# Kernel optimization log

Hardware: AMD Instinct MI355X
Metric: run time of the kernel (lower is better)

Reference implementation:

```python
import jax, jax.numpy as jnp
import numpy as np

K = 9          # neighbors kept after dilation
DILATION = 2   # top-k runs with K*DILATION then strided slice
EPS = 1e-12    # F.normalize eps


def setup_inputs() -> dict:
    key = jax.random.key(0)
    # x: [B, C, N, 1] feature map over N points with C channels
    x = jax.random.normal(key, (2, 64, 8192, 1), dtype=jnp.float32)
    return {"x": x}


def reference(x):
    k_total = K * DILATION
    # L2-normalize along channel dim (F.normalize(x, p=2, dim=1))
    norm = jnp.sqrt(jnp.sum(x * x, axis=1, keepdims=True))
    xn = x / jnp.maximum(norm, EPS)
    # [B, C, N, 1] -> [B, N, C]
    pts = jnp.transpose(jnp.squeeze(xn, -1), (0, 2, 1))
    B, N, _ = pts.shape
    # pairwise squared distances: ||xi||^2 - 2 xi.xj + ||xj||^2  -> [B, N, N]
    sq = jnp.sum(pts * pts, axis=-1, keepdims=True)            # [B, N, 1]
    dist = sq - 2.0 * jnp.einsum('bnc,bmc->bnm', pts, pts) + jnp.swapaxes(sq, 1, 2)
    # k nearest = top-k of negated distance (matches torch.topk(-dist, k))
    _, nn_idx = jax.lax.top_k(-dist, k_total)                  # [B, N, k_total] int32
    center_idx = jnp.broadcast_to(jnp.arange(N, dtype=nn_idx.dtype)[None, :, None],
                                  (B, N, k_total))
    edge_index = jnp.stack([nn_idx, center_idx], axis=0)       # [2, B, N, k_total]
    # dilation (non-stochastic path): strided slice over neighbor dim
    return edge_index[:, :, :, ::DILATION]                     # [2, B, N, K]
```

## Files before the change

kernel.cpp:

```cpp
#include <hip/hip_runtime.h>


#define NPTS  8192
#define CHN   64
#define NB    2
#define KF    18
#define KC    8
#define KM    16
#define KOUT  9
#define NPART 4
#define TPB   32

typedef unsigned u32;
typedef unsigned short u16;
typedef unsigned long long u64;
typedef __attribute__((ext_vector_type(4))) unsigned u32x4;
typedef __attribute__((ext_vector_type(8))) short bf16x8;
typedef __attribute__((ext_vector_type(4))) float f32x4;

__device__ __forceinline__ u32 umin32(u32 a, u32 b) { return a < b ? a : b; }

__device__ __forceinline__ u32 mono32(float f) {
  const u32 u = __float_as_uint(f);
  const u32 s = (u32)((int)u >> 31);
  return u ^ (s | 0x80000000u);
}

__device__ __forceinline__ u32 med3u(u32 a, u32 b, u32 c) {
  u32 r;
  asm("v_med3_u32 %0, %1, %2, %3" : "=v"(r) : "v"(a), "v"(b), "v"(c));
  return r;
}

template <int KK>
__device__ __forceinline__ void insmm(u32 key, u32 (&d)[KK]) {
#pragma unroll
  for (int k = KK - 1; k >= 1; --k) d[k] = med3u(d[k - 1], d[k], key);
  d[0] = umin32(d[0], key);
}

template <int KK>
__device__ __forceinline__ void ins64(u64 key, u64 (&d)[KK]) {
  if (key < d[KK - 1]) {
#pragma unroll
    for (int k = KK - 1; k >= 1; --k) {
      const bool up = d[k - 1] > key;
      const bool here = (!up) && (d[k] > key);
      d[k] = up ? d[k - 1] : (here ? key : d[k]);
    }
    if (d[0] > key) d[0] = key;
  }
}

__device__ __forceinline__ void gload_lds16(const u32* g, u32* l) {
  __builtin_amdgcn_global_load_lds(
      (const __attribute__((address_space(1))) u32*)g,
      (__attribute__((address_space(3))) u32*)l, 16, 0, 0);
}

__device__ __forceinline__ void np_normalize(const float* __restrict__ xb,
                                             float (&v)[CHN]) {
  float ss = 0.f;
#pragma unroll
  for (int c = 0; c < CHN; ++c) {
    v[c] = xb[(size_t)c * NPTS];
    ss = __fadd_rn(ss, __fmul_rn(v[c], v[c]));
  }
  const float den = fmaxf(__fsqrt_rn(ss), 1e-12f);
#pragma unroll
  for (int c = 0; c < CHN; ++c) v[c] = __fdiv_rn(v[c], den);
}

__global__ __launch_bounds__(128) void prep_kernel(
    const float* __restrict__ x, u32* __restrict__ hib, u32* __restrict__ lob,
    u32* __restrict__ w16b, float* __restrict__ sq) {
  const int b = blockIdx.x >> 6;
  const int n = ((blockIdx.x & 63) << 7) + threadIdx.x;
  const int g = (b << 13) + n;
  float v[CHN];
  np_normalize(x + (size_t)b * CHN * NPTS + n, v);
  float r[8];
#pragma unroll
  for (int j = 0; j < 8; ++j) r[j] = __fmul_rn(v[j], v[j]);
#pragma unroll
  for (int blk = 1; blk < 8; ++blk)
#pragma unroll
    for (int j = 0; j < 8; ++j)
      r[j] = __fadd_rn(r[j], __fmul_rn(v[8 * blk + j], v[8 * blk + j]));
  const float t0 = __fadd_rn(r[0], r[1]);
  const float t1 = __fadd_rn(r[2], r[3]);
  const float t2 = __fadd_rn(r[4], r[5]);
  const float t3 = __fadd_rn(r[6], r[7]);
  sq[g] = __fadd_rn(__fadd_rn(t0, t1), __fadd_rn(t2, t3));
  u32* hd = hib + (size_t)g * 32;
  u32* ld = lob + (size_t)g * 32;
  u32* wd = w16b + (size_t)g * 32;
  const int key = n & 7;
#pragma unroll
  for (int q = 0; q < 8; ++q) {
    u32 h[4], l[4], w[4];
#pragma unroll
    for (int p2 = 0; p2 < 4; ++p2) {
      const float a = v[8 * q + 2 * p2];
      const float c = v[8 * q + 2 * p2 + 1];
      const u32 ba = __float_as_uint(a), bc = __float_as_uint(c);
      const float la = a - __uint_as_float(ba & 0xffff0000u);
      const float lc = c - __uint_as_float(bc & 0xffff0000u);
      h[p2] = __builtin_amdgcn_perm(bc, ba, 0x07060302u);
      l[p2] = __builtin_amdgcn_perm(__float_as_uint(lc), __float_as_uint(la),
                                    0x07060302u);
      w[p2] = __builtin_amdgcn_perm(bc, ba, 0x05040100u);
    }
    const int pq = (q ^ key) << 2;
    *(u32x4*)(hd + pq) = (u32x4){h[0], h[1], h[2], h[3]};
    *(u32x4*)(ld + pq) = (u32x4){l[0], l[1], l[2], l[3]};
    *(u32x4*)(wd + pq) = (u32x4){w[0], w[1], w[2], w[3]};
  }
}

__global__ __launch_bounds__(256, 2) void knn_part_kernel(
    const u32* __restrict__ hib, const u32* __restrict__ lob,
    const float* __restrict__ sq, u16* __restrict__ cand) {
  __shared__ __align__(16) u32 pw[4][2][2048];

  const int tid = threadIdx.x;
  const int vb = ((blockIdx.x & 7) << 7) + (blockIdx.x >> 3);
  const int part = vb >> 8;
  const int w = vb & 255;
  const int b = w >> 7;
  const int qbase = (w & 127) << 6;
  const int t_lo = part << 5;
  const u32* __restrict__ hb_ = hib + ((size_t)b << 18);
  const u32* __restrict__ lb_ = lob + ((size_t)b << 18);
  const float* __restrict__ sqb = sq + (b << 13);

  const int lane = tid & 63, wid = tid >> 6;
  const int qoff = (wid & 1) << 5;
  const int moff = (wid >> 1) << 5;
  const int l15 = lane & 15;
  const int h4 = lane >> 4;
  const int sw = l15 & 7;
  const int lofs = lane << 2;

#define STAGE(BUF, TILE)                                                     \
  {                                                                          \
    const u32* sH_ = hb_ + ((size_t)(TILE) << 11) + (moff << 5);             \
    const u32* sL_ = lb_ + ((size_t)(TILE) << 11) + (moff << 5);             \
    u32* bp_ = &pw[wid][(BUF)][0];                                           \
    gload_lds16(sH_ + lofs, bp_ + lofs);                                     \
    gload_lds16(sH_ + 256 + lofs, bp_ + 256 + lofs);                         \
    gload_lds16(sH_ + 512 + lofs, bp_ + 512 + lofs);                         \
    gload_lds16(sH_ + 768 + lofs, bp_ + 768 + lofs);                         \
    gload_lds16(sL_ + lofs, bp_ + 1024 + lofs);                              \
    gload_lds16(sL_ + 256 + lofs, bp_ + 1280 + lofs);                        \
    gload_lds16(sL_ + 512 + lofs, bp_ + 1536 + lofs);                        \
    gload_lds16(sL_ + 768 + lofs, bp_ + 1792 + lofs);                        \
  }

  STAGE(0, t_lo)
  float sqn0 = sqb[(t_lo << 6) + moff + l15];
  float sqn1 = sqb[(t_lo << 6) + moff + 16 + l15];

  bf16x8 ah[2][2], al[2][2];
#pragma unroll
  for (int g = 0; g < 2; ++g)
#pragma unroll
    for (int s = 0; s < 2; ++s) {
      const int row = qbase + qoff + (g << 4) + l15;
      const int off = row * 32 + ((((s << 2) + h4) ^ sw) << 2);
      u32x4 hv = *(const u32x4*)(hb_ + off);
      u32x4 lv = *(const u32x4*)(lb_ + off);
      hv.x ^= 0x80008000u; hv.y ^= 0x80008000u;
      hv.z ^= 0x80008000u; hv.w ^= 0x80008000u;
      lv.x ^= 0x80008000u; lv.y ^= 0x80008000u;
      lv.z ^= 0x80008000u; lv.w ^= 0x80008000u;
      ah[g][s] = __builtin_bit_cast(bf16x8, hv);
      al[g][s] = __builtin_bit_cast(bf16x8, lv);
    }
  asm volatile("s_waitcnt vmcnt(0)" ::: "memory");
  __builtin_amdgcn_sched_barrier(0);

  u32 d[2][4][KC];
#pragma unroll
  for (int g = 0; g < 2; ++g)
#pragma unroll
    for (int i = 0; i < 4; ++i)
#pragma unroll
      for (int k = 0; k < KC; ++k) d[g][i][k] = 0xffffffffu;

  for (int tau = 0; tau < TPB; ++tau) {
    const int cur = tau & 1;
    const float sq0 = sqn0, sq1 = sqn1;
    if (tau + 1 < TPB) {
      STAGE(cur ^ 1, t_lo + tau + 1)
      sqn0 = sqb[((t_lo + tau + 1) << 6) + moff + l15];
      sqn1 = sqb[((t_lo + tau + 1) << 6) + moff + 16 + l15];
      asm volatile("s_waitcnt vmcnt(10)" ::: "memory");
    } else {
      asm volatile("s_waitcnt vmcnt(0)" ::: "memory");
    }
    __builtin_amdgcn_sched_barrier(0);

    const u32* ppc = &pw[wid][cur][0];
#pragma unroll
    for (int f = 0; f < 2; ++f) {
      const float sqm = ((f ? sq1 : sq0) + 2.f) * 0.5f;
      const int rloc = (f << 4) + l15;
      f32x4 acc[2];
      acc[0] = (f32x4){sqm, sqm, sqm, sqm};
      acc[1] = acc[0];
#pragma unroll
      for (int s = 0; s < 2; ++s) {
        const u32* hp = ppc + rloc * 32 + ((((s << 2) + h4) ^ sw) << 2);
        const bf16x8 bh = __builtin_bit_cast(bf16x8, *(const u32x4*)hp);
        const bf16x8 bl = __builtin_bit_cast(bf16x8, *(const u32x4*)(hp + 1024));
        acc[0] = __builtin_amdgcn_mfma_f32_16x16x32_bf16(ah[0][s], bh, acc[0], 0, 0, 0);
        acc[1] = __builtin_amdgcn_mfma_f32_16x16x32_bf16(ah[1][s], bh, acc[1], 0, 0, 0);
        acc[0] = __builtin_amdgcn_mfma_f32_16x16x32_bf16(al[0][s], bh, acc[0], 0, 0, 0);
        acc[1] = __builtin_amdgcn_mfma_f32_16x16x32_bf16(al[1][s], bh, acc[1], 0, 0, 0);
        acc[0] = __builtin_amdgcn_mfma_f32_16x16x32_bf16(ah[0][s], bl, acc[0], 0, 0, 0);
        acc[1] = __builtin_amdgcn_mfma_f32_16x16x32_bf16(ah[1][s], bl, acc[1], 0, 0, 0);
      }
      const u32 lidx = (u32)((tau << 6) + moff + rloc);
#pragma unroll
      for (int g = 0; g < 2; ++g)
#pragma unroll
        for (int i = 0; i < 4; ++i) {
          const u32 keyv = (__float_as_uint(acc[g][i]) & 0xfffff000u) | lidx;
          insmm<KC>(keyv, d[g][i]);
        }
    }
  }
#undef STAGE
  __syncthreads();

  u32* dmp = &pw[0][0][0];
  u32* m1b = dmp + 8448;
  u32* m2b = dmp + 12144;
  const int stream = ((wid >> 1) << 4) + l15;
  const int rcb = ((wid & 1) << 4) + (h4 << 2);
#pragma unroll
  for (int chunk = 0; chunk < 2; ++chunk) {
#pragma unroll
    for (int i = 0; i < 4; ++i) {
      const int col = stream * 33 + rcb + i;
#pragma unroll
      for (int k = 0; k < KC; ++k) dmp[k * 1056 + col] = d[chunk][i][k];
    }
    __syncthreads();
    {
      const int rowc = tid >> 3, oct = tid & 7;
      u32 m1[14];
#pragma unroll
      for (int k = 0; k < 14; ++k) m1[k] = 0xffffffffu;
#pragma unroll
      for (int s = 0; s < 4; ++s) {
        const int col = (oct * 4 + s) * 33 + rowc;
#pragma unroll
        for (int j = 0; j < KC; ++j) insmm<14>(dmp[j * 1056 + col], m1);
      }
      const int col = oct * 33 + rowc;
#pragma unroll
      for (int k = 0; k < 14; ++k) m1b[k * 264 + col] = m1[k];
    }
    __syncthreads();
    if (tid < 64) {
      const int rowc = tid >> 1, half = tid & 1;
      u32 m2[KM];
#pragma unroll
      for (int k = 0; k < KM; ++k) m2[k] = 0xffffffffu;
#pragma unroll
      for (int o = 0; o < 4; ++o) {
        const int col = (half * 4 + o) * 33 + rowc;
#pragma unroll
        for (int j = 0; j < 14; ++j) insmm<KM>(m1b[j * 264 + col], m2);
      }
      const int col = half * 33 + rowc;
#pragma unroll
      for (int k = 0; k < KM; ++k) m2b[k * 66 + col] = m2[k];
    }
    __syncthreads();
    if (tid < 32) {
      u32 m3[KM];
#pragma unroll
      for (int k = 0; k < KM; ++k) m3[k] = 0xffffffffu;
#pragma unroll
      for (int h = 0; h < 2; ++h) {
        const int col = h * 33 + tid;
#pragma unroll
        for (int k = 0; k < KM; ++k) insmm<KM>(m2b[k * 66 + col], m3);
      }
      const int row = ((tid >> 4) << 5) + (chunk << 4) + (tid & 15);
      const int rg = (b << 13) + qbase + row;
      u16* cw = cand + (size_t)rg * (NPART * KM) + part * KM;
#pragma unroll
      for (int k = 0; k < KM; ++k)
        cw[k] = (u16)((part << 11) + (m3[k] & 0xfffu));
    }
    __syncthreads();
  }
}

__global__ __launch_bounds__(512) void finalize_kernel(
    const u32* __restrict__ hib, const u32* __restrict__ w16b,
    const float* __restrict__ sq, const u16* __restrict__ cand,
    int* __restrict__ out) {
  __shared__ u64 ex[64 * 66];
  __shared__ u64 hf[128 * 19];
  const int tid = threadIdx.x;
  const int rl = tid >> 3, sub = tid & 7;
  const int row = (blockIdx.x << 6) + rl;
  const int b = row >> 13;
  const int n = row & 8191;
  const float sqn = sq[row];
  const float* __restrict__ sqb = sq + (b << 13);
  const u32* __restrict__ hb_ = hib + ((size_t)b << 18);
  const u32* __restrict__ wb_ = w16b + ((size_t)b << 18);
  float vq[CHN];
  {
    const u32* hq = hb_ + ((size_t)n << 5);
    const u32* wq = wb_ + ((size_t)n << 5);
    const int key = n & 7;
#pragma unroll
    for (int q = 0; q < 8; ++q) {
      const int pq = (q ^ key) << 2;
      const u32x4 hw = *(const u32x4*)(hq + pq);
      const u32x4 ww = *(const u32x4*)(wq + pq);
      const u32 hv[4] = {hw.x, hw.y, hw.z, hw.w};
      const u32 wv[4] = {ww.x, ww.y, ww.z, ww.w};
#pragma unroll
      for (int p2 = 0; p2 < 4; ++p2) {
        vq[8 * q + 2 * p2] =
            __uint_as_float((hv[p2] << 16) | (wv[p2] & 0xffffu));
        vq[8 * q + 2 * p2 + 1] =
            __uint_as_float((hv[p2] & 0xffff0000u) | (wv[p2] >> 16));
      }
    }
  }
  const u16* __restrict__ cr = cand + (size_t)row * 64 + sub * 8;
  u64* exw = ex + rl * 66 + sub * 8;
  for (int j = 0; j < 8; ++j) {
    const int ix = cr[j];
    const u32* hp = hb_ + ((size_t)ix << 5);
    const u32* wp = wb_ + ((size_t)ix << 5);
    const int key = ix & 7;
    float dot = 0.f;
#pragma unroll
    for (int q = 0; q < 8; ++q) {
      const int pq = (q ^ key) << 2;
      const u32x4 hw = *(const u32x4*)(hp + pq);
      const u32x4 ww = *(const u32x4*)(wp + pq);
      const u32 hv[4] = {hw.x, hw.y, hw.z, hw.w};
      const u32 wv[4] = {ww.x, ww.y, ww.z, ww.w};
#pragma unroll
      for (int p2 = 0; p2 < 4; ++p2) {
        const float a = __uint_as_float((hv[p2] << 16) | (wv[p2] & 0xffffu));
        const float c = __uint_as_float((hv[p2] & 0xffff0000u) | (wv[p2] >> 16));
        dot = __fadd_rn(dot, __fmul_rn(vq[8 * q + 2 * p2], a));
        dot = __fadd_rn(dot, __fmul_rn(vq[8 * q + 2 * p2 + 1], c));
      }
    }
    const float dist =
        __fadd_rn(__fsub_rn(sqn, __fmul_rn(2.0f, dot)), sqb[ix]);
    exw[j] = ((u64)mono32(dist) << 32) | (u32)ix;
  }
  __syncthreads();
  if (tid < 128) {
    const int r2 = tid >> 1, hv = tid & 1;
    u64 m18[KF];
#pragma unroll
    for (int k = 0; k < KF; ++k) m18[k] = ~0ull;
    const u64* p = ex + r2 * 66 + hv * 32;
    for (int j = 0; j < 32; ++j) ins64<KF>(p[j], m18);
    u64* wr = hf + tid * 19;
#pragma unroll
    for (int k = 0; k < KF; ++k) wr[k] = m18[k];
  }
  __syncthreads();
  if (tid < 64) {
    u64 m18[KF];
#pragma unroll
    for (int k = 0; k < KF; ++k) m18[k] = ~0ull;
    const u64* p0 = hf + (tid << 1) * 19;
    const u64* p1 = hf + ((tid << 1) + 1) * 19;
    for (int j = 0; j < KF; ++j) ins64<KF>(p0[j], m18);
    for (int j = 0; j < KF; ++j) ins64<KF>(p1[j], m18);
    const int row2 = (blockIdx.x << 6) + tid;
    int* o0 = out + (size_t)row2 * KOUT;
    int* o1 = o0 + NB * NPTS * KOUT;
#pragma unroll
    for (int k = 0; k < KOUT; ++k) {
      o0[k] = (int)(m18[2 * k] & 0xffffffffu);
      o1[k] = row2 & 8191;
    }
  }
}

extern "C" void kernel_launch(void* const* d_in, const int* in_sizes, int n_in,
                              void* d_out, int out_size, void* d_ws, size_t ws_size,
                              hipStream_t stream) {
  const float* x = (const float*)d_in[0];
  u32* hib = (u32*)d_ws;
  u32* lob = hib + (size_t)NB * NPTS * 32;
  u32* w16b = lob + (size_t)NB * NPTS * 32;
  float* sqg = (float*)(w16b + (size_t)NB * NPTS * 32);
  u16* cand = (u16*)(sqg + NB * NPTS);
  int* out = (int*)d_out;
  prep_kernel<<<dim3(128), dim3(128), 0, stream>>>(x, hib, lob, w16b, sqg);
  knn_part_kernel<<<dim3(1024), dim3(256), 0, stream>>>(hib, lob, sqg, cand);
  finalize_kernel<<<dim3(256), dim3(512), 0, stream>>>(hib, w16b, sqg, cand, out);
}
```

Baseline: 202.0 us.

## Drop bf16 low-part split in candidate MFMA pass, widen candidate list

```diff
diff --git a/kernel.cpp b/kernel.cpp
--- a/kernel.cpp
+++ b/kernel.cpp
@@ -6,7 +6,8 @@
 #define NB    2
 #define KF    18
 #define KC    8
-#define KM    16
+#define KM    20
+#define KM1   16
 #define KOUT  9
 #define NPART 4
 #define TPB   32
@@ -72,7 +73,7 @@
 }
 
 __global__ __launch_bounds__(128) void prep_kernel(
-    const float* __restrict__ x, u32* __restrict__ hib, u32* __restrict__ lob,
+    const float* __restrict__ x, u32* __restrict__ hib,
     u32* __restrict__ w16b, float* __restrict__ sq) {
   const int b = blockIdx.x >> 6;
   const int n = ((blockIdx.x & 63) << 7) + threadIdx.x;
@@ -93,35 +94,28 @@
   const float t3 = __fadd_rn(r[6], r[7]);
   sq[g] = __fadd_rn(__fadd_rn(t0, t1), __fadd_rn(t2, t3));
   u32* hd = hib + (size_t)g * 32;
-  u32* ld = lob + (size_t)g * 32;
   u32* wd = w16b + (size_t)g * 32;
   const int key = n & 7;
 #pragma unroll
   for (int q = 0; q < 8; ++q) {
-    u32 h[4], l[4], w[4];
+    u32 h[4], w[4];
 #pragma unroll
     for (int p2 = 0; p2 < 4; ++p2) {
-      const float a = v[8 * q + 2 * p2];
-      const float c = v[8 * q + 2 * p2 + 1];
-      const u32 ba = __float_as_uint(a), bc = __float_as_uint(c);
-      const float la = a - __uint_as_float(ba & 0xffff0000u);
-      const float lc = c - __uint_as_float(bc & 0xffff0000u);
+      const u32 ba = __float_as_uint(v[8 * q + 2 * p2]);
+      const u32 bc = __float_as_uint(v[8 * q + 2 * p2 + 1]);
       h[p2] = __builtin_amdgcn_perm(bc, ba, 0x07060302u);
-      l[p2] = __builtin_amdgcn_perm(__float_as_uint(lc), __float_as_uint(la),
-                                    0x07060302u);
       w[p2] = __builtin_amdgcn_perm(bc, ba, 0x05040100u);
     }
     const int pq = (q ^ key) << 2;
     *(u32x4*)(hd + pq) = (u32x4){h[0], h[1], h[2], h[3]};
-    *(u32x4*)(ld + pq) = (u32x4){l[0], l[1], l[2], l[3]};
     *(u32x4*)(wd + pq) = (u32x4){w[0], w[1], w[2], w[3]};
   }
 }
 
-__global__ __launch_bounds__(256, 2) void knn_part_kernel(
-    const u32* __restrict__ hib, const u32* __restrict__ lob,
-    const float* __restrict__ sq, u16* __restrict__ cand) {
-  __shared__ __align__(16) u32 pw[4][2][2048];
+__global__ __launch_bounds__(256, 3) void knn_part_kernel(
+    const u32* __restrict__ hib, const float* __restrict__ sq,
+    u16* __restrict__ cand) {
+  __shared__ __align__(16) u32 smem[12672];
 
   const int tid = threadIdx.x;
   const int vb = ((blockIdx.x & 7) << 7) + (blockIdx.x >> 3);
@@ -131,7 +125,6 @@
   const int qbase = (w & 127) << 6;
   const int t_lo = part << 5;
   const u32* __restrict__ hb_ = hib + ((size_t)b << 18);
-  const u32* __restrict__ lb_ = lob + ((size_t)b << 18);
   const float* __restrict__ sqb = sq + (b << 13);
 
   const int lane = tid & 63, wid = tid >> 6;
@@ -141,27 +134,23 @@
   const int h4 = lane >> 4;
   const int sw = l15 & 7;
   const int lofs = lane << 2;
+  u32* wstage = smem + (wid << 11);
 
 #define STAGE(BUF, TILE)                                                     \
   {                                                                          \
     const u32* sH_ = hb_ + ((size_t)(TILE) << 11) + (moff << 5);             \
-    const u32* sL_ = lb_ + ((size_t)(TILE) << 11) + (moff << 5);             \
-    u32* bp_ = &pw[wid][(BUF)][0];                                           \
+    u32* bp_ = wstage + ((BUF) << 10);                                       \
     gload_lds16(sH_ + lofs, bp_ + lofs);                                     \
     gload_lds16(sH_ + 256 + lofs, bp_ + 256 + lofs);                         \
     gload_lds16(sH_ + 512 + lofs, bp_ + 512 + lofs);                         \
     gload_lds16(sH_ + 768 + lofs, bp_ + 768 + lofs);                         \
-    gload_lds16(sL_ + lofs, bp_ + 1024 + lofs);                              \
-    gload_lds16(sL_ + 256 + lofs, bp_ + 1280 + lofs);                        \
-    gload_lds16(sL_ + 512 + lofs, bp_ + 1536 + lofs);                        \
-    gload_lds16(sL_ + 768 + lofs, bp_ + 1792 + lofs);                        \
   }
 
   STAGE(0, t_lo)
   float sqn0 = sqb[(t_lo << 6) + moff + l15];
   float sqn1 = sqb[(t_lo << 6) + moff + 16 + l15];
 
-  bf16x8 ah[2][2], al[2][2];
+  bf16x8 ah[2][2];
 #pragma unroll
   for (int g = 0; g < 2; ++g)
 #pragma unroll
@@ -169,13 +158,9 @@
       const int row = qbase + qoff + (g << 4) + l15;
       const int off = row * 32 + ((((s << 2) + h4) ^ sw) << 2);
       u32x4 hv = *(const u32x4*)(hb_ + off);
-      u32x4 lv = *(const u32x4*)(lb_ + off);
       hv.x ^= 0x80008000u; hv.y ^= 0x80008000u;
       hv.z ^= 0x80008000u; hv.w ^= 0x80008000u;
-      lv.x ^= 0x80008000u; lv.y ^= 0x80008000u;
-      lv.z ^= 0x80008000u; lv.w ^= 0x80008000u;
       ah[g][s] = __builtin_bit_cast(bf16x8, hv);
-      al[g][s] = __builtin_bit_cast(bf16x8, lv);
     }
   asm volatile("s_waitcnt vmcnt(0)" ::: "memory");
   __builtin_amdgcn_sched_barrier(0);
@@ -195,13 +180,13 @@
       STAGE(cur ^ 1, t_lo + tau + 1)
       sqn0 = sqb[((t_lo + tau + 1) << 6) + moff + l15];
       sqn1 = sqb[((t_lo + tau + 1) << 6) + moff + 16 + l15];
-      asm volatile("s_waitcnt vmcnt(10)" ::: "memory");
+      asm volatile("s_waitcnt vmcnt(6)" ::: "memory");
     } else {
       asm volatile("s_waitcnt vmcnt(0)" ::: "memory");
     }
     __builtin_amdgcn_sched_barrier(0);
 
-    const u32* ppc = &pw[wid][cur][0];
+    const u32* ppc = wstage + (cur << 10);
 #pragma unroll
     for (int f = 0; f < 2; ++f) {
       const float sqm = ((f ? sq1 : sq0) + 2.f) * 0.5f;
@@ -213,13 +198,8 @@
       for (int s = 0; s < 2; ++s) {
         const u32* hp = ppc + rloc * 32 + ((((s << 2) + h4) ^ sw) << 2);
         const bf16x8 bh = __builtin_bit_cast(bf16x8, *(const u32x4*)hp);
-        const bf16x8 bl = __builtin_bit_cast(bf16x8, *(const u32x4*)(hp + 1024));
         acc[0] = __builtin_amdgcn_mfma_f32_16x16x32_bf16(ah[0][s], bh, acc[0], 0, 0, 0);
         acc[1] = __builtin_amdgcn_mfma_f32_16x16x32_bf16(ah[1][s], bh, acc[1], 0, 0, 0);
-        acc[0] = __builtin_amdgcn_mfma_f32_16x16x32_bf16(al[0][s], bh, acc[0], 0, 0, 0);
-        acc[1] = __builtin_amdgcn_mfma_f32_16x16x32_bf16(al[1][s], bh, acc[1], 0, 0, 0);
-        acc[0] = __builtin_amdgcn_mfma_f32_16x16x32_bf16(ah[0][s], bl, acc[0], 0, 0, 0);
-        acc[1] = __builtin_amdgcn_mfma_f32_16x16x32_bf16(ah[1][s], bl, acc[1], 0, 0, 0);
       }
       const u32 lidx = (u32)((tau << 6) + moff + rloc);
 #pragma unroll
@@ -234,9 +214,9 @@
 #undef STAGE
   __syncthreads();
 
-  u32* dmp = &pw[0][0][0];
-  u32* m1b = dmp + 8448;
-  u32* m2b = dmp + 12144;
+  u32* dmp = smem;
+  u32* m1b = smem + 8448;
+  u32* m2b = smem;
   const int stream = ((wid >> 1) << 4) + l15;
   const int rcb = ((wid & 1) << 4) + (h4 << 2);
 #pragma unroll
@@ -250,18 +230,18 @@
     __syncthreads();
     {
       const int rowc = tid >> 3, oct = tid & 7;
-      u32 m1[14];
-#pragma unroll
-      for (int k = 0; k < 14; ++k) m1[k] = 0xffffffffu;
+      u32 m1[KM1];
+#pragma unroll
+      for (int k = 0; k < KM1; ++k) m1[k] = 0xffffffffu;
 #pragma unroll
       for (int s = 0; s < 4; ++s) {
         const int col = (oct * 4 + s) * 33 + rowc;
 #pragma unroll
-        for (int j = 0; j < KC; ++j) insmm<14>(dmp[j * 1056 + col], m1);
+        for (int j = 0; j < KC; ++j) insmm<KM1>(dmp[j * 1056 + col], m1);
       }
       const int col = oct * 33 + rowc;
 #pragma unroll
-      for (int k = 0; k < 14; ++k) m1b[k * 264 + col] = m1[k];
+      for (int k = 0; k < KM1; ++k) m1b[k * 264 + col] = m1[k];
     }
     __syncthreads();
     if (tid < 64) {
@@ -273,7 +253,7 @@
       for (int o = 0; o < 4; ++o) {
         const int col = (half * 4 + o) * 33 + rowc;
 #pragma unroll
-        for (int j = 0; j < 14; ++j) insmm<KM>(m1b[j * 264 + col], m2);
+        for (int j = 0; j < KM1; ++j) insmm<KM>(m1b[j * 264 + col], m2);
       }
       const int col = half * 33 + rowc;
 #pragma unroll
@@ -305,7 +285,7 @@
     const u32* __restrict__ hib, const u32* __restrict__ w16b,
     const float* __restrict__ sq, const u16* __restrict__ cand,
     int* __restrict__ out) {
-  __shared__ u64 ex[64 * 66];
+  __shared__ u64 ex[64 * 81];
   __shared__ u64 hf[128 * 19];
   const int tid = threadIdx.x;
   const int rl = tid >> 3, sub = tid & 7;
@@ -337,9 +317,9 @@
       }
     }
   }
-  const u16* __restrict__ cr = cand + (size_t)row * 64 + sub * 8;
-  u64* exw = ex + rl * 66 + sub * 8;
-  for (int j = 0; j < 8; ++j) {
+  const u16* __restrict__ cr = cand + (size_t)row * 80 + sub * 10;
+  u64* exw = ex + rl * 81 + sub * 10;
+  for (int j = 0; j < 10; ++j) {
     const int ix = cr[j];
     const u32* hp = hb_ + ((size_t)ix << 5);
     const u32* wp = wb_ + ((size_t)ix << 5);
@@ -370,8 +350,8 @@
     u64 m18[KF];
 #pragma unroll
     for (int k = 0; k < KF; ++k) m18[k] = ~0ull;
-    const u64* p = ex + r2 * 66 + hv * 32;
-    for (int j = 0; j < 32; ++j) ins64<KF>(p[j], m18);
+    const u64* p = ex + r2 * 81 + hv * 40;
+    for (int j = 0; j < 40; ++j) ins64<KF>(p[j], m18);
     u64* wr = hf + tid * 19;
 #pragma unroll
     for (int k = 0; k < KF; ++k) wr[k] = m18[k];
@@ -401,12 +381,11 @@
                               hipStream_t stream) {
   const float* x = (const float*)d_in[0];
   u32* hib = (u32*)d_ws;
-  u32* lob = hib + (size_t)NB * NPTS * 32;
-  u32* w16b = lob + (size_t)NB * NPTS * 32;
+  u32* w16b = hib + (size_t)NB * NPTS * 32;
   float* sqg = (float*)(w16b + (size_t)NB * NPTS * 32);
   u16* cand = (u16*)(sqg + NB * NPTS);
   int* out = (int*)d_out;
-  prep_kernel<<<dim3(128), dim3(128), 0, stream>>>(x, hib, lob, w16b, sqg);
-  knn_part_kernel<<<dim3(1024), dim3(256), 0, stream>>>(hib, lob, sqg, cand);
+  prep_kernel<<<dim3(128), dim3(128), 0, stream>>>(x, hib, w16b, sqg);
+  knn_part_kernel<<<dim3(1024), dim3(256), 0, stream>>>(hib, sqg, cand);
   finalize_kernel<<<dim3(256), dim3(512), 0, stream>>>(hib, w16b, sqg, cand, out);
 }
```

Result: slower. 219.8 us (+8.8%).
